# Kernel tuning notes

Hardware: AMD Instinct MI355X
Metric: run time of the kernel (lower is better)

Reference implementation:

```python
import jax, jax.numpy as jnp
import numpy as np

B, SQ, SKV, D, H, DH, P = 8, 2048, 2048, 1024, 8, 128, 1024
LN_EPS = 1e-3  # keras LayerNormalization default


def _glorot(key, shape):
    fan_in, fan_out = shape[-2], shape[-1]
    lim = np.sqrt(6.0 / (fan_in + fan_out))
    return jax.random.uniform(key, shape, jnp.float32, -lim, lim)


def _layernorm(x, gamma, beta, eps=LN_EPS):
    mu = jnp.mean(x, axis=-1, keepdims=True)
    var = jnp.mean(jnp.square(x - mu), axis=-1, keepdims=True)
    return (x - mu) * jax.lax.rsqrt(var + eps) * gamma + beta


def setup_inputs() -> dict:
    key = jax.random.key(0)
    ks = jax.random.split(key, 8)
    return {
        "query": jax.random.normal(ks[0], (B, SQ, D), jnp.float32),
        "value": jax.random.normal(ks[1], (B, SKV, D), jnp.float32),
        "W1": _glorot(ks[2], (H, D, DH)),   # per-head query proj (stacked)
        "W2": _glorot(ks[3], (H, D, DH)),   # per-head key proj
        "W3": _glorot(ks[4], (H, D, DH)),   # per-head value proj
        "Wp": _glorot(ks[5], (H * DH, P)),  # output projection
        "bp": jnp.zeros((P,), jnp.float32),
        "Wt": _glorot(ks[6], (P, P)),       # transform (relu FFN)
        "bt": jnp.zeros((P,), jnp.float32),
        "g1": jnp.ones((P,), jnp.float32),
        "b1": jnp.zeros((P,), jnp.float32),
        "g2": jnp.ones((P,), jnp.float32),
        "b2": jnp.zeros((P,), jnp.float32),
    }


def reference(query, value, W1, W2, W3, Wp, bp, Wt, bt, g1, b1, g2, b2):
    # batched multi-head attention (original loops over heads; math identical)
    q = jnp.einsum("bsd,hde->bhse", query, W1)   # [B,H,SQ,DH]
    k = jnp.einsum("btd,hde->bhte", value, W2)   # [B,H,SKV,DH]
    v = jnp.einsum("btd,hde->bhte", value, W3)   # [B,H,SKV,DH]
    scale = 1.0 / jnp.sqrt(jnp.asarray(DH, jnp.float32))
    scores = jnp.einsum("bhse,bhte->bhst", q, k) * scale
    attn = jax.nn.softmax(scores, axis=-1)
    ctx = jnp.einsum("bhst,bhte->bhse", attn, v)  # [B,H,SQ,DH]
    # concat heads along feature axis
    cat = ctx.transpose(0, 2, 1, 3).reshape(B, SQ, H * DH)
    # project + residual + layernorm (dropout inactive: rate=0 / inference)
    proj = cat @ Wp + bp + query
    proj = _layernorm(proj, g1, b1)
    # relu transform + residual + layernorm
    t = jax.nn.relu(proj @ Wt + bt) + proj
    return _layernorm(t, g2, b2)
```

## Files before the change

kernel.cpp:

```cpp
#include <hip/hip_runtime.h>
#include <hip/hip_bf16.h>


typedef __bf16 bf16x8 __attribute__((ext_vector_type(8)));
typedef float  f32x4  __attribute__((ext_vector_type(4)));
typedef float  f32x16 __attribute__((ext_vector_type(16)));
typedef unsigned u32x4 __attribute__((ext_vector_type(4)));

#define GLDS16(g, l)                                                         \
  __builtin_amdgcn_global_load_lds(                                          \
      (__attribute__((address_space(1))) void*)(g),                          \
      (__attribute__((address_space(3))) void*)(l), 16, 0, 0)

__device__ __forceinline__ unsigned short f2bfu(float f) {
  unsigned int u = __builtin_bit_cast(unsigned int, f);
  u += 0x7fffu + ((u >> 16) & 1u);
  return (unsigned short)(u >> 16);
}
__device__ __forceinline__ float bfu2f(unsigned short u) {
  return __builtin_bit_cast(float, (unsigned int)u << 16);
}

__global__ __launch_bounds__(256) void cast2_f32_bf16(
    const float* __restrict__ in0, unsigned short* __restrict__ out0,
    const float* __restrict__ in1, unsigned short* __restrict__ out1, int n) {
  const float* in = blockIdx.z ? in1 : in0;
  unsigned short* out = blockIdx.z ? out1 : out0;
  int i = (blockIdx.x * 256 + threadIdx.x) * 4;
  int stride = gridDim.x * 256 * 4;
  for (; i < n; i += stride) {
    float4 v = *(const float4*)(in + i);
    ushort4 o;
    o.x = f2bfu(v.x); o.y = f2bfu(v.y); o.z = f2bfu(v.z); o.w = f2bfu(v.w);
    *(ushort4*)(out + i) = o;
  }
}

__device__ __forceinline__ void tc_body(const float* in, unsigned short* out,
                                        int R, int C) {
  __shared__ float tile[32][33];
  int tx = threadIdx.x, ty = threadIdx.y;
  int c0 = blockIdx.x * 32, r0 = blockIdx.y * 32;
#pragma unroll
  for (int j = 0; j < 4; j++)
    tile[ty + j * 8][tx] = in[(size_t)(r0 + ty + j * 8) * C + c0 + tx];
  __syncthreads();
#pragma unroll
  for (int j = 0; j < 4; j++)
    out[(size_t)(c0 + ty + j * 8) * R + r0 + tx] = f2bfu(tile[tx][ty + j * 8]);
}

__global__ __launch_bounds__(256) void transpose_heads(
    const float* __restrict__ W1, const float* __restrict__ W2,
    const float* __restrict__ W3, unsigned short* __restrict__ O1,
    unsigned short* __restrict__ O2, unsigned short* __restrict__ O3) {
  int z = blockIdx.z, t = z >> 3, s = z & 7;
  const float* in = (t == 0 ? W1 : t == 1 ? W2 : W3) + (size_t)s * 1024 * 128;
  unsigned short* out = (t == 0 ? O1 : t == 1 ? O2 : O3) + (size_t)s * 1024 * 128;
  tc_body(in, out, 1024, 128);
}

__global__ __launch_bounds__(256) void transpose_sq(
    const float* __restrict__ Wp, const float* __restrict__ Wt,
    unsigned short* __restrict__ Op, unsigned short* __restrict__ Ot) {
  const float* in = blockIdx.z ? Wt : Wp;
  unsigned short* out = blockIdx.z ? Ot : Op;
  tc_body(in, out, 1024, 1024);
}

template <int MODE>
__global__ __launch_bounds__(512, 2) void gemm256(
    const unsigned short* __restrict__ A, const unsigned short* __restrict__ Bt,
    void* __restrict__ out, const float* __restrict__ bias,
    const void* __restrict__ extra, float scale, float scale1,
    long strideA, long strideB, long strideO, int ntiles) {
  int bz = blockIdx.z;
  A  += (size_t)bz * strideA;
  Bt += (size_t)bz * strideB;
  float sc = bz ? scale1 : scale;
  int nb = gridDim.x;
  int qq = nb >> 3;
  int lin = blockIdx.x;
  int sw = (lin & 7) * qq + (lin >> 3);
  int nt = sw % ntiles, mt = sw / ntiles;
  int m0 = mt * 256, n0 = nt * 256;
  int tid = threadIdx.x;
  int wid = tid >> 6, lane = tid & 63;
  int l15 = lane & 15, l4 = lane >> 4;
  int wm = (wid >> 2) * 128, wn = (wid & 3) * 64;

  __shared__ alignas(16) char lds[131072];

  f32x4 acc[8][4];
#pragma unroll
  for (int i = 0; i < 8; i++)
#pragma unroll
    for (int j = 0; j < 4; j++) acc[i][j] = (f32x4){0.f, 0.f, 0.f, 0.f};

  const char* gA = (const char*)A + (size_t)m0 * 2048;
  const char* gB = (const char*)Bt + (size_t)n0 * 2048;

  auto STAGE = [&](int buf, int t) {
    char* ab = lds + buf * 65536;
    char* bb = ab + 32768;
#pragma unroll
    for (int i = 0; i < 4; i++) {
      int s = i * 512 + tid;
      int row = s >> 3;
      int g = (s & 7) ^ (row & 7);
      unsigned dst = (unsigned)((i * 512 + (tid & ~63)) * 16);
      GLDS16(gA + (size_t)row * 2048 + t * 128 + g * 16, ab + dst);
      GLDS16(gB + (size_t)row * 2048 + t * 128 + g * 16, bb + dst);
    }
  };

  STAGE(0, 0);
  for (int t = 0; t < 16; t++) {
    __builtin_amdgcn_sched_barrier(0);
    __builtin_amdgcn_s_barrier();
    if (t < 15) {
      STAGE((t + 1) & 1, t + 1);
      asm volatile("s_waitcnt vmcnt(8)" ::: "memory");
    } else {
      asm volatile("s_waitcnt vmcnt(0)" ::: "memory");
    }
    __builtin_amdgcn_s_barrier();
    __builtin_amdgcn_sched_barrier(0);

    const char* ab = lds + (t & 1) * 65536;
    const char* bb = ab + 32768;
#pragma unroll
    for (int kk = 0; kk < 2; kk++) {
      bf16x8 bfr[4];
#pragma unroll
      for (int nf = 0; nf < 4; nf++) {
        int r = wn + nf * 16 + l15;
        bfr[nf] = *(const bf16x8*)(bb + r * 128 + (((kk * 4 + l4) ^ (r & 7)) << 4));
      }
#pragma unroll
      for (int mh = 0; mh < 2; mh++) {
        bf16x8 af[4];
#pragma unroll
        for (int mf = 0; mf < 4; mf++) {
          int r = wm + mh * 64 + mf * 16 + l15;
          af[mf] = *(const bf16x8*)(ab + r * 128 + (((kk * 4 + l4) ^ (r & 7)) << 4));
        }
        __builtin_amdgcn_s_setprio(1);
#pragma unroll
        for (int mf = 0; mf < 4; mf++)
#pragma unroll
          for (int nf = 0; nf < 4; nf++)
            acc[mh * 4 + mf][nf] = __builtin_amdgcn_mfma_f32_16x16x32_bf16(
                af[mf], bfr[nf], acc[mh * 4 + mf][nf], 0, 0, 0);
        __builtin_amdgcn_s_setprio(0);
      }
    }
  }

  unsigned short* outp = (unsigned short*)out + (size_t)bz * strideO;
#pragma unroll
  for (int mi = 0; mi < 8; mi++)
#pragma unroll
    for (int nf = 0; nf < 4; nf++)
#pragma unroll
      for (int r = 0; r < 4; r++) {
        int gm = m0 + wm + mi * 16 + l4 * 4 + r;
        int gn = n0 + wn + nf * 16 + l15;
        float v = acc[mi][nf][r];
        if constexpr (MODE == 0) {
          int b = gm >> 11, s = gm & 2047, h = gn >> 7, e = gn & 127;
          outp[((((size_t)b * 8 + h) * 2048 + s) << 7) + e] = f2bfu(v * sc);
        } else if constexpr (MODE == 1) {
          outp[(size_t)gm * 2048 + gn] = f2bfu(v);
        } else if constexpr (MODE == 2) {
          float r2 = v + bias[gn] + ((const float*)extra)[(size_t)gm * 1024 + gn];
          outp[(size_t)gm * 1024 + gn] = f2bfu(r2);
        } else {
          float pl = bfu2f(((const unsigned short*)extra)[(size_t)gm * 1024 + gn]);
          outp[(size_t)gm * 1024 + gn] = f2bfu(fmaxf(v + bias[gn], 0.0f) + pl);
        }
      }
}

__global__ __launch_bounds__(512) void fa_kernel(
    const unsigned short* __restrict__ Qh,
    const unsigned short* __restrict__ Kh,
    const unsigned short* __restrict__ Vt,
    unsigned short* __restrict__ catO) {
  int h = blockIdx.x, qt = blockIdx.y, b = blockIdx.z;
  int tid = threadIdx.x, wid = tid >> 6, lane = tid & 63;
  int q31 = lane & 31, hi = lane >> 5;

  __shared__ alignas(16) char lds[131072];

  const char* gK = (const char*)(Kh + (((size_t)b * 8 + h) * 2048) * 128);
  const char* gV = (const char*)(Vt + ((size_t)b * 1024 + h * 128) * 2048);

  bf16x8 qf[8];
  {
    const char* gQ = (const char*)(Qh + (((size_t)b * 8 + h) * 2048
                        + (size_t)qt * 256 + wid * 32 + q31) * 128);
#pragma unroll
    for (int ks = 0; ks < 8; ks++)
      qf[ks] = *(const bf16x8*)(gQ + ks * 32 + hi * 16);
  }

  f32x16 o[4];
#pragma unroll
  for (int et = 0; et < 4; et++)
#pragma unroll
    for (int r = 0; r < 16; r++) o[et][r] = 0.f;
  float lacc0 = 0.f, lacc1 = 0.f;

  auto STAGE_K = [&](int kt) {
    char* kb = lds + (kt & 3) * 16384;
#pragma unroll
    for (int pass = 0; pass < 2; pass++) {
      int c = pass * 512 + tid;
      int row = c >> 4, ch = c & 15;
      int g = ch ^ (row & 15);
      GLDS16(gK + (size_t)(kt * 64 + row) * 256 + g * 16,
             kb + (pass * 512 + (tid & ~63)) * 16);
    }
  };
  auto STAGE_V = [&](int kt) {
    char* vb = lds + 65536 + (kt & 3) * 16384;
#pragma unroll
    for (int pass = 0; pass < 2; pass++) {
      int c = pass * 512 + tid;
      int row = c >> 4, g = c & 15;
      int gp = g ^ (row & 15);
      int e = ((gp >> 3) << 6) + row;
      GLDS16(gV + (size_t)e * 4096 + kt * 128 + (gp & 7) * 16,
             vb + (pass * 512 + (tid & ~63)) * 16);
    }
  };
  auto QK = [&](int kt, f32x16& r0, f32x16& r1) {
    const char* kb = lds + (kt & 3) * 16384;
#pragma unroll
    for (int r = 0; r < 16; r++) { r0[r] = 0.f; r1[r] = 0.f; }
#pragma unroll
    for (int ks = 0; ks < 8; ks++) {
      int g = ((2 * ks + hi) ^ (q31 & 15)) << 4;
      bf16x8 k0 = *(const bf16x8*)(kb + q31 * 256 + g);
      bf16x8 k1 = *(const bf16x8*)(kb + (q31 + 32) * 256 + g);
      r0 = __builtin_amdgcn_mfma_f32_32x32x16_bf16(k0, qf[ks], r0, 0, 0, 0);
      r1 = __builtin_amdgcn_mfma_f32_32x32x16_bf16(k1, qf[ks], r1, 0, 0, 0);
    }
  };
  auto SOFT_PV = [&](int kt, f32x16& s0, f32x16& s1) {
    float p[32];
#pragma unroll
    for (int r = 0; r < 16; r++) p[r] = __builtin_amdgcn_exp2f(s0[r]);
#pragma unroll
    for (int r = 0; r < 16; r++) p[16 + r] = __builtin_amdgcn_exp2f(s1[r]);
#pragma unroll
    for (int r = 0; r < 16; r++) { lacc0 += p[r]; lacc1 += p[16 + r]; }
    bf16x8 pa[4];
#pragma unroll
    for (int g = 0; g < 4; g++) {
      unsigned a0, a1, b0, b1;
      float p0 = p[g * 8 + 0], p1 = p[g * 8 + 1], p2 = p[g * 8 + 2], p3 = p[g * 8 + 3];
      float p4 = p[g * 8 + 4], p5 = p[g * 8 + 5], p6 = p[g * 8 + 6], p7 = p[g * 8 + 7];
      asm("v_cvt_pk_bf16_f32 %0, %1, %2" : "=v"(a0) : "v"(p0), "v"(p1));
      asm("v_cvt_pk_bf16_f32 %0, %1, %2" : "=v"(b0) : "v"(p4), "v"(p5));
      asm("v_cvt_pk_bf16_f32 %0, %1, %2" : "=v"(a1) : "v"(p2), "v"(p3));
      asm("v_cvt_pk_bf16_f32 %0, %1, %2" : "=v"(b1) : "v"(p6), "v"(p7));
      asm volatile("v_permlane32_swap_b32 %0, %1" : "+v"(a0), "+v"(b0));
      asm volatile("v_permlane32_swap_b32 %0, %1" : "+v"(a1), "+v"(b1));
      u32x4 w; w[0] = a0; w[1] = a1; w[2] = b0; w[3] = b1;
      pa[g] = __builtin_bit_cast(bf16x8, w);
    }
    const char* vb = lds + 65536 + (kt & 3) * 16384;
#pragma unroll
    for (int et = 0; et < 4; et++) {
      int row = (et & 1) * 32 + q31;
      int gb = (et >> 1) * 8;
#pragma unroll
      for (int ks = 0; ks < 4; ks++) {
        bf16x8 vf = *(const bf16x8*)(vb + row * 256 +
                        (((gb + 2 * ks + hi) ^ (row & 15)) << 4));
        o[et] = __builtin_amdgcn_mfma_f32_32x32x16_bf16(vf, pa[ks], o[et], 0, 0, 0);
      }
    }
  };

  STAGE_K(0); STAGE_V(0); STAGE_K(1); STAGE_V(1);

  for (int w = 0; w < 16; w++) {
    int kt = 2 * w;
    asm volatile("s_waitcnt lgkmcnt(0)" ::: "memory");
    __builtin_amdgcn_sched_barrier(0);
    __builtin_amdgcn_s_barrier();
    if (w < 15) {
      STAGE_K(kt + 2); STAGE_V(kt + 2); STAGE_K(kt + 3); STAGE_V(kt + 3);
      asm volatile("s_waitcnt vmcnt(8)" ::: "memory");
    } else {
      asm volatile("s_waitcnt vmcnt(0)" ::: "memory");
    }
    __builtin_amdgcn_s_barrier();
    __builtin_amdgcn_sched_barrier(0);
    f32x16 sA0, sA1, sB0, sB1;
    QK(kt, sA0, sA1);
    QK(kt + 1, sB0, sB1);
    SOFT_PV(kt, sA0, sA1);
    SOFT_PV(kt + 1, sB0, sB1);
  }

  float lacc = lacc0 + lacc1;
  lacc += __shfl_xor(lacc, 32);
  float linv = 1.0f / lacc;
  __syncthreads();
  char* reg = lds + wid * 8192;
  int swz = (lane & 7) << 4;
#pragma unroll
  for (int et = 0; et < 4; et++)
#pragma unroll
    for (int pr = 0; pr < 8; pr++) {
      float lo = o[et][2 * pr] * linv, hf = o[et][2 * pr + 1] * linv;
      unsigned w;
      asm("v_cvt_pk_bf16_f32 %0, %1, %2" : "=v"(w) : "v"(lo), "v"(hf));
      int e = et * 32 + 8 * (pr >> 1) + 4 * hi + (pr & 1) * 2;
      *(unsigned*)(reg + q31 * 256 + ((e * 2) ^ swz)) = w;
    }
  size_t orow = (size_t)b * 2048 + (size_t)qt * 256 + wid * 32;
#pragma unroll
  for (int pass = 0; pass < 8; pass++) {
    int n = pass * 64 + lane;
    int q = n >> 4, ch = n & 15;
    bf16x8 v = *(const bf16x8*)(reg + q * 256 + ((ch * 16) ^ ((q & 7) << 4)));
    *(bf16x8*)((char*)(catO + (orow + q) * 1024 + h * 128) + ch * 16) = v;
  }
}

template <int IN_BF16, int OUT_BF16>
__global__ __launch_bounds__(256) void ln_kernel(
    const void* __restrict__ in, const float* __restrict__ g,
    const float* __restrict__ be, void* __restrict__ out) {
  int row = blockIdx.x;
  int tid = threadIdx.x;
  float4 v;
  if constexpr (IN_BF16) {
    ushort4 u = ((const ushort4*)in)[(size_t)row * 256 + tid];
    v.x = bfu2f(u.x); v.y = bfu2f(u.y); v.z = bfu2f(u.z); v.w = bfu2f(u.w);
  } else {
    v = ((const float4*)in)[(size_t)row * 256 + tid];
  }
  float s = v.x + v.y + v.z + v.w;
  float sq = v.x * v.x + v.y * v.y + v.z * v.z + v.w * v.w;
#pragma unroll
  for (int m = 1; m < 64; m <<= 1) {
    s += __shfl_xor(s, m);
    sq += __shfl_xor(sq, m);
  }
  __shared__ float ws[8];
  int wid = tid >> 6, lane = tid & 63;
  if (lane == 0) { ws[wid] = s; ws[wid + 4] = sq; }
  __syncthreads();
  s = ws[0] + ws[1] + ws[2] + ws[3];
  sq = ws[4] + ws[5] + ws[6] + ws[7];
  float mu = s * (1.0f / 1024.0f);
  float var = sq * (1.0f / 1024.0f) - mu * mu;
  float rs = rsqrtf(var + 1e-3f);
  float4 gg = ((const float4*)g)[tid];
  float4 bb = ((const float4*)be)[tid];
  float y0 = (v.x - mu) * rs * gg.x + bb.x;
  float y1 = (v.y - mu) * rs * gg.y + bb.y;
  float y2 = (v.z - mu) * rs * gg.z + bb.z;
  float y3 = (v.w - mu) * rs * gg.w + bb.w;
  if constexpr (OUT_BF16) {
    ushort4 ov;
    ov.x = f2bfu(y0); ov.y = f2bfu(y1); ov.z = f2bfu(y2); ov.w = f2bfu(y3);
    ((ushort4*)out)[(size_t)row * 256 + tid] = ov;
  } else {
    float4 ov = {y0, y1, y2, y3};
    ((float4*)out)[(size_t)row * 256 + tid] = ov;
  }
}

extern "C" void kernel_launch(void* const* d_in, const int* in_sizes, int n_in,
                              void* d_out, int out_size, void* d_ws, size_t ws_size,
                              hipStream_t stream) {
  const float* query = (const float*)d_in[0];
  const float* value = (const float*)d_in[1];
  const float* W1 = (const float*)d_in[2];
  const float* W2 = (const float*)d_in[3];
  const float* W3 = (const float*)d_in[4];
  const float* Wp = (const float*)d_in[5];
  const float* bp = (const float*)d_in[6];
  const float* Wt = (const float*)d_in[7];
  const float* bt = (const float*)d_in[8];
  const float* g1 = (const float*)d_in[9];
  const float* b1 = (const float*)d_in[10];
  const float* g2 = (const float*)d_in[11];
  const float* b2 = (const float*)d_in[12];

  char* ws = (char*)d_ws;
  unsigned short* qbf  = (unsigned short*)(ws + 0);
  unsigned short* vbf  = (unsigned short*)(ws + 33554432);
  unsigned short* Qh   = (unsigned short*)(ws + 67108864);
  unsigned short* Kh   = (unsigned short*)(ws + 100663296);
  unsigned short* Vt   = (unsigned short*)(ws + 134217728);
  unsigned short* Wq_t = (unsigned short*)(ws + 167772160);
  unsigned short* Wk_t = (unsigned short*)(ws + 169869312);
  unsigned short* Wv_t = (unsigned short*)(ws + 171966464);
  unsigned short* Wp_t = (unsigned short*)(ws + 174063616);
  unsigned short* Wt_t = (unsigned short*)(ws + 176160768);
  unsigned short* cat_  = qbf;
  unsigned short* projb = Qh;
  unsigned short* pln   = vbf;
  unsigned short* tb    = Kh;

  const int NE = 16384 * 1024;
  cast2_f32_bf16<<<dim3(2048, 1, 2), 256, 0, stream>>>(query, qbf, value, vbf, NE);

  dim3 tbk(32, 8);
  transpose_heads<<<dim3(4, 32, 24), tbk, 0, stream>>>(W1, W2, W3, Wq_t, Wk_t, Wv_t);
  transpose_sq<<<dim3(32, 32, 2), tbk, 0, stream>>>(Wp, Wt, Wp_t, Wt_t);

  const float QSCALE = 0.08838834764831845f * 1.4426950408889634f;
  gemm256<0><<<dim3(256, 1, 2), 512, 0, stream>>>(
      qbf, Wq_t, Qh, nullptr, nullptr, QSCALE, 1.0f,
      16777216L, 1048576L, 16777216L, 4);
  gemm256<1><<<dim3(32, 1, 8), 512, 0, stream>>>(
      Wv_t, vbf, Vt, nullptr, nullptr, 1.0f, 1.0f,
      0, 2048L * 1024L, 1024L * 2048L, 8);
  fa_kernel<<<dim3(8, 8, 8), 512, 0, stream>>>(Qh, Kh, Vt, cat_);
  gemm256<2><<<dim3(256, 1, 1), 512, 0, stream>>>(
      cat_, Wp_t, projb, bp, query, 1.0f, 1.0f, 0, 0, 0, 4);
  ln_kernel<1, 1><<<16384, 256, 0, stream>>>(projb, g1, b1, pln);
  gemm256<3><<<dim3(256, 1, 1), 512, 0, stream>>>(
      pln, Wt_t, tb, bt, pln, 1.0f, 1.0f, 0, 0, 0, 4);
  ln_kernel<1, 0><<<16384, 256, 0, stream>>>(tb, g2, b2, (float*)d_out);
}
```

Before: 409.8 us.

## Split GEMM mainloop into four barrier-fenced load/MFMA phases per k-tile

Restructures the bf16 GEMM inner loop. B fragments for both k-substeps are now loaded once per tile. A fragments are loaded in four phases of two m-fragments each, and each phase is fenced by s_barrier, lgkmcnt(0) and a trailing barrier around its MFMA burst. The barrier at the top of the tile loop is removed, because the trailing per-phase barrier now protects the double buffer against being overwritten while still being read. The aim is to keep waves in lockstep so LDS reads and MFMA bursts interleave across waves. The cost is more barriers per tile and full LDS waits before each MFMA group.

Result: slower. 419.1 us (+2.3%).

```diff
diff --git a/kernel.cpp b/kernel.cpp
--- a/kernel.cpp
+++ b/kernel.cpp
@@ -117,7 +117,6 @@
   STAGE(0, 0);
   for (int t = 0; t < 16; t++) {
     __builtin_amdgcn_sched_barrier(0);
-    __builtin_amdgcn_s_barrier();
     if (t < 15) {
       STAGE((t + 1) & 1, t + 1);
       asm volatile("s_waitcnt vmcnt(8)" ::: "memory");
@@ -129,31 +128,43 @@
 
     const char* ab = lds + (t & 1) * 65536;
     const char* bb = ab + 32768;
-#pragma unroll
-    for (int kk = 0; kk < 2; kk++) {
-      bf16x8 bfr[4];
-#pragma unroll
-      for (int nf = 0; nf < 4; nf++) {
-        int r = wn + nf * 16 + l15;
-        bfr[nf] = *(const bf16x8*)(bb + r * 128 + (((kk * 4 + l4) ^ (r & 7)) << 4));
+    bf16x8 bfr[4][2];
+#pragma unroll
+    for (int p = 0; p < 4; p++) {
+      if (p == 0) {
+#pragma unroll
+        for (int nf = 0; nf < 4; nf++)
+#pragma unroll
+          for (int kk = 0; kk < 2; kk++) {
+            int r = wn + nf * 16 + l15;
+            bfr[nf][kk] = *(const bf16x8*)(bb + r * 128 +
+                              (((kk * 4 + l4) ^ (r & 7)) << 4));
+          }
       }
-#pragma unroll
-      for (int mh = 0; mh < 2; mh++) {
-        bf16x8 af[4];
-#pragma unroll
-        for (int mf = 0; mf < 4; mf++) {
-          int r = wm + mh * 64 + mf * 16 + l15;
-          af[mf] = *(const bf16x8*)(ab + r * 128 + (((kk * 4 + l4) ^ (r & 7)) << 4));
+      bf16x8 af[2][2];
+#pragma unroll
+      for (int mf2 = 0; mf2 < 2; mf2++)
+#pragma unroll
+        for (int kk = 0; kk < 2; kk++) {
+          int r = wm + (p * 2 + mf2) * 16 + l15;
+          af[mf2][kk] = *(const bf16x8*)(ab + r * 128 +
+                            (((kk * 4 + l4) ^ (r & 7)) << 4));
         }
-        __builtin_amdgcn_s_setprio(1);
-#pragma unroll
-        for (int mf = 0; mf < 4; mf++)
-#pragma unroll
-          for (int nf = 0; nf < 4; nf++)
-            acc[mh * 4 + mf][nf] = __builtin_amdgcn_mfma_f32_16x16x32_bf16(
-                af[mf], bfr[nf], acc[mh * 4 + mf][nf], 0, 0, 0);
-        __builtin_amdgcn_s_setprio(0);
-      }
+      __builtin_amdgcn_s_barrier();
+      asm volatile("s_waitcnt lgkmcnt(0)" ::: "memory");
+      __builtin_amdgcn_sched_barrier(0);
+      __builtin_amdgcn_s_setprio(1);
+#pragma unroll
+      for (int mf2 = 0; mf2 < 2; mf2++)
+#pragma unroll
+        for (int nf = 0; nf < 4; nf++)
+#pragma unroll
+          for (int kk = 0; kk < 2; kk++)
+            acc[p * 2 + mf2][nf] = __builtin_amdgcn_mfma_f32_16x16x32_bf16(
+                af[mf2][kk], bfr[nf][kk], acc[p * 2 + mf2][nf], 0, 0, 0);
+      __builtin_amdgcn_s_setprio(0);
+      __builtin_amdgcn_sched_barrier(0);
+      __builtin_amdgcn_s_barrier();
     }
   }
 
```
